# Performance work log

Hardware: AMD Instinct MI355X
Metric: run time of the kernel (lower is better)

## Reference

```python
import jax, jax.numpy as jnp
import numpy as np

B, T, F, U = 256, 2048, 64, 64
KEEP = 0.5  # recurrent_dropout=0.5 -> keep prob 0.5


def setup_inputs() -> dict:
    key = jax.random.key(0)
    ks = jax.random.split(key, 7)
    inputs = jax.random.normal(ks[0], (B, T, F), dtype=jnp.float32)
    kernel = jax.random.normal(ks[1], (F, 3 * U), dtype=jnp.float32) * 0.1
    recurrent_kernel = jax.random.normal(ks[2], (U, 3 * U), dtype=jnp.float32) * 0.1
    bias = jax.random.normal(ks[3], (2, 3 * U), dtype=jnp.float32) * 0.1
    dense_w = jax.random.normal(ks[4], (U, 1), dtype=jnp.float32) * 0.1
    dense_b = jnp.zeros((1,), dtype=jnp.float32)
    # Keras recurrent dropout: one fixed mask per gate (z, r, h), constant over time,
    # applied to h_prev before the recurrent matmul; inverted-dropout scaling.
    bern = jax.random.bernoulli(ks[5], KEEP, (3, B, U)).astype(jnp.float32)
    rec_mask = bern / KEEP
    return {
        "inputs": inputs,
        "kernel": kernel,
        "recurrent_kernel": recurrent_kernel,
        "bias": bias,
        "dense_w": dense_w,
        "dense_b": dense_b,
        "rec_mask": rec_mask,
    }


def _gru_dense(inputs, kernel, recurrent_kernel, bias, dense_w, dense_b, rec_mask):
    # Precompute input projections for all timesteps: [B, T, 3U]
    x_proj = jnp.einsum("btf,fg->btg", inputs, kernel) + bias[0]
    Uz, Ur, Uh = jnp.split(recurrent_kernel, 3, axis=1)  # each [U, U]
    bz, br, bh = jnp.split(bias[1], 3)                   # each [U]
    mz, mr, mh = rec_mask[0], rec_mask[1], rec_mask[2]   # each [B, U]

    def step(h, xt):
        xz, xr, xh = jnp.split(xt, 3, axis=-1)  # each [B, U]
        z = jax.nn.sigmoid(xz + (h * mz) @ Uz + bz)
        r = jax.nn.sigmoid(xr + (h * mr) @ Ur + br)
        hh = jnp.tanh(xh + r * ((h * mh) @ Uh + bh))  # reset_after=True
        h_new = z * h + (1.0 - z) * hh
        return h_new, None

    h0 = jnp.zeros((B, U), dtype=inputs.dtype)
    h_last, _ = jax.lax.scan(step, h0, jnp.swapaxes(x_proj, 0, 1))  # scan over T
    return h_last @ dense_w + dense_b  # [B, 1]


def reference(inputs, kernel, recurrent_kernel, bias, dense_w, dense_b, rec_mask):
    return _gru_dense(inputs, kernel, recurrent_kernel, bias, dense_w, dense_b, rec_mask)
```

## Files before the change

### kernel.cpp

```cpp
#include <hip/hip_runtime.h>

#define BB 256
#define TT 2048
#define FF 64
#define UU 64
#define C3 192

__device__ __forceinline__ float readlane_f(float v, int lane) {
    return __int_as_float(__builtin_amdgcn_readlane(__float_as_int(v), lane));
}
__device__ __forceinline__ float fast_sigmoid(float x) {
    return __builtin_amdgcn_rcpf(1.0f + __expf(-x));
}
__device__ __forceinline__ float fast_tanh(float x) {
    return 1.0f - 2.0f * __builtin_amdgcn_rcpf(__expf(2.0f * x) + 1.0f);
}

#define REP16(M) M(0) M(1) M(2) M(3) M(4) M(5) M(6) M(7) \
                 M(8) M(9) M(10) M(11) M(12) M(13) M(14) M(15)

__global__ __launch_bounds__(256, 1)
void gru_coop(const float* __restrict__ in, const float* __restrict__ kmat,
              const float* __restrict__ rk, const float* __restrict__ bias,
              const float* __restrict__ mask, const float* __restrict__ dw,
              const float* __restrict__ db, float* __restrict__ out) {
    __shared__ float ps[2][4][64][5];
    const int b    = blockIdx.x;
    const int lane = threadIdx.x & 63;
    const int wv   = threadIdx.x >> 6;
    const int i0   = wv << 4;

    const float mzv = mask[(size_t)b * UU + lane];
    const float mrv = mask[(size_t)(BB * UU) + (size_t)b * UU + lane];
    const float mhv = mask[(size_t)(2 * BB * UU) + (size_t)b * UU + lane];

#define DECLW(I) float uz_##I, ur_##I, uh_##I, kz_##I, kr_##I, kh_##I;
    REP16(DECLW)
#define INITW(I) { const int i_ = i0 + (I); \
    uz_##I = rk[i_ * C3 + lane]        * readlane_f(mzv, i_); \
    ur_##I = rk[i_ * C3 + 64 + lane]   * readlane_f(mrv, i_); \
    uh_##I = rk[i_ * C3 + 128 + lane]  * readlane_f(mhv, i_); \
    kz_##I = kmat[i_ * C3 + lane]; \
    kr_##I = kmat[i_ * C3 + 64 + lane]; \
    kh_##I = kmat[i_ * C3 + 128 + lane]; }
    REP16(INITW)

    const float bzf = bias[lane]       + bias[C3 + lane];
    const float brf = bias[64 + lane]  + bias[C3 + 64 + lane];
    const float bh0 = bias[128 + lane];
    const float bh1 = bias[C3 + 128 + lane];

    const float* __restrict__ inb = in + (size_t)b * TT * FF;

    float a0 = inb[(size_t)0 * FF + lane];
    float a1 = inb[(size_t)1 * FF + lane];
    float a2 = inb[(size_t)2 * FF + lane];
    float a3 = inb[(size_t)3 * FF + lane];
    float n0, n1, n2, n3;

    float h = 0.0f;

#define ACC1(I, AV) { \
    const float hs_ = readlane_f(h,  i0 + (I)); \
    const float as_ = readlane_f(AV, i0 + (I)); \
    pz  = fmaf(hs_, uz_##I, pz);  pz  = fmaf(as_, kz_##I, pz); \
    pr  = fmaf(hs_, ur_##I, pr);  pr  = fmaf(as_, kr_##I, pr); \
    pah = fmaf(hs_, uh_##I, pah); pxh = fmaf(as_, kh_##I, pxh); }

#define SUBSTEP(S, AV, NV) { \
    const int t_ = (tb << 2) + (S); \
    { const int rn_ = (t_ + 4 < TT) ? (t_ + 4) : (TT - 1); \
      NV = inb[(size_t)rn_ * FF + lane]; } \
    float pz = 0.0f, pr = 0.0f, pxh = 0.0f, pah = 0.0f; \
    REP16(ACC_##AV) \
    float* wp_ = &ps[(S) & 1][wv][lane][0]; \
    wp_[0] = pz; wp_[1] = pr; wp_[2] = pxh; wp_[3] = pah; \
    __syncthreads(); \
    float sz = bzf, sr = brf, sxh = bh0, sah = bh1; \
    { const float* rp_ = &ps[(S) & 1][0][lane][0]; \
      sz += rp_[0];   sr += rp_[1];   sxh += rp_[2];   sah += rp_[3]; \
      sz += rp_[320]; sr += rp_[321]; sxh += rp_[322]; sah += rp_[323]; \
      sz += rp_[640]; sr += rp_[641]; sxh += rp_[642]; sah += rp_[643]; \
      sz += rp_[960]; sr += rp_[961]; sxh += rp_[962]; sah += rp_[963]; } \
    const float z_  = fast_sigmoid(sz); \
    const float r_  = fast_sigmoid(sr); \
    const float hh_ = fast_tanh(fmaf(r_, sah, sxh)); \
    h = fmaf(z_, h - hh_, hh_); }

#define ACC_a0(I) ACC1(I, a0)
#define ACC_a1(I) ACC1(I, a1)
#define ACC_a2(I) ACC1(I, a2)
#define ACC_a3(I) ACC1(I, a3)

#pragma unroll 1
    for (int tb = 0; tb < TT / 4; ++tb) {
        SUBSTEP(0, a0, n0)
        SUBSTEP(1, a1, n1)
        SUBSTEP(2, a2, n2)
        SUBSTEP(3, a3, n3)
        a0 = n0; a1 = n1; a2 = n2; a3 = n3;
    }

    if (wv == 0) {
        float p = h * dw[lane];
#pragma unroll
        for (int o = 32; o > 0; o >>= 1) p += __shfl_down(p, o, 64);
        if (lane == 0) out[b] = p + db[0];
    }
}

extern "C" void kernel_launch(void* const* d_in, const int* in_sizes, int n_in,
                              void* d_out, int out_size, void* d_ws, size_t ws_size,
                              hipStream_t stream) {
    const float* inputs = (const float*)d_in[0];
    const float* kmat   = (const float*)d_in[1];
    const float* rk     = (const float*)d_in[2];
    const float* bias   = (const float*)d_in[3];
    const float* dw     = (const float*)d_in[4];
    const float* db     = (const float*)d_in[5];
    const float* mask   = (const float*)d_in[6];
    float* out = (float*)d_out;

    gru_coop<<<BB, 256, 0, stream>>>(inputs, kmat, rk, bias, mask, dw, db, out);
}
```

Before: 939.6 us.

## Repartition GRU step by output units with shuffle reduction and LDS h broadcast

Each wave now owns 16 output units, and the 64 lanes split the 64-term contraction into four 16-term groups. Partials are combined with cross-lane xor shuffles instead of an LDS reduction, and the new hidden state is broadcast through a double-buffered LDS array read as float4. Inputs are prefetched by one wave into an LDS ring. The aim is to cut the per-step readlane chain and the LDS reduction traffic, at the cost of shuffle latency and an extra LDS read of h each step.

```diff
diff --git a/kernel.cpp b/kernel.cpp
--- a/kernel.cpp
+++ b/kernel.cpp
@@ -6,103 +6,130 @@
 #define UU 64
 #define C3 192
 
-__device__ __forceinline__ float readlane_f(float v, int lane) {
-    return __int_as_float(__builtin_amdgcn_readlane(__float_as_int(v), lane));
-}
 __device__ __forceinline__ float fast_sigmoid(float x) {
     return __builtin_amdgcn_rcpf(1.0f + __expf(-x));
 }
 __device__ __forceinline__ float fast_tanh(float x) {
     return 1.0f - 2.0f * __builtin_amdgcn_rcpf(__expf(2.0f * x) + 1.0f);
 }
+__device__ __forceinline__ float shflx(float v, int m) {
+    return __shfl_xor(v, m, 64);
+}
 
 #define REP16(M) M(0) M(1) M(2) M(3) M(4) M(5) M(6) M(7) \
                  M(8) M(9) M(10) M(11) M(12) M(13) M(14) M(15)
 
-__global__ __launch_bounds__(256, 1)
-void gru_coop(const float* __restrict__ in, const float* __restrict__ kmat,
-              const float* __restrict__ rk, const float* __restrict__ bias,
-              const float* __restrict__ mask, const float* __restrict__ dw,
-              const float* __restrict__ db, float* __restrict__ out) {
-    __shared__ float ps[2][4][64][5];
+__global__ void __launch_bounds__(256)
+__attribute__((amdgpu_waves_per_eu(1, 1)))
+gru_v4(const float* __restrict__ in, const float* __restrict__ kmat,
+       const float* __restrict__ rk, const float* __restrict__ bias,
+       const float* __restrict__ mask, const float* __restrict__ dw,
+       const float* __restrict__ db, float* __restrict__ out) {
+    __shared__ __align__(16) float hbuf[2][64];
+    __shared__ __align__(16) float abuf[8][64];
+
     const int b    = blockIdx.x;
     const int lane = threadIdx.x & 63;
     const int wv   = threadIdx.x >> 6;
-    const int i0   = wv << 4;
+    const int sub  = lane >> 4;
+    const int u    = lane & 15;
+    const int j    = wv * 16 + u;
+    const int i0   = sub * 16;
 
-    const float mzv = mask[(size_t)b * UU + lane];
-    const float mrv = mask[(size_t)(BB * UU) + (size_t)b * UU + lane];
-    const float mhv = mask[(size_t)(2 * BB * UU) + (size_t)b * UU + lane];
-
-#define DECLW(I) float uz_##I, ur_##I, uh_##I, kz_##I, kr_##I, kh_##I;
+    const float* mzp = mask;
+    const float* mrp = mask + (size_t)BB * UU;
+    const float* mhp = mask + (size_t)2 * BB * UU;
+#define DECLW(K) float uz##K, ur##K, uh##K, kz##K, kr##K, kh##K;
     REP16(DECLW)
-#define INITW(I) { const int i_ = i0 + (I); \
-    uz_##I = rk[i_ * C3 + lane]        * readlane_f(mzv, i_); \
-    ur_##I = rk[i_ * C3 + 64 + lane]   * readlane_f(mrv, i_); \
-    uh_##I = rk[i_ * C3 + 128 + lane]  * readlane_f(mhv, i_); \
-    kz_##I = kmat[i_ * C3 + lane]; \
-    kr_##I = kmat[i_ * C3 + 64 + lane]; \
-    kh_##I = kmat[i_ * C3 + 128 + lane]; }
+#define INITW(K) { const int i_ = i0 + (K); \
+    uz##K = rk[i_ * C3 + j]        * mzp[(size_t)b * UU + i_]; \
+    ur##K = rk[i_ * C3 + 64 + j]   * mrp[(size_t)b * UU + i_]; \
+    uh##K = rk[i_ * C3 + 128 + j]  * mhp[(size_t)b * UU + i_]; \
+    kz##K = kmat[i_ * C3 + j]; \
+    kr##K = kmat[i_ * C3 + 64 + j]; \
+    kh##K = kmat[i_ * C3 + 128 + j]; }
     REP16(INITW)
 
-    const float bzf = bias[lane]       + bias[C3 + lane];
-    const float brf = bias[64 + lane]  + bias[C3 + 64 + lane];
-    const float bh0 = bias[128 + lane];
-    const float bh1 = bias[C3 + 128 + lane];
+    const float bzj  = bias[j]       + bias[C3 + j];
+    const float brj  = bias[64 + j]  + bias[C3 + 64 + j];
+    const float bh0j = bias[128 + j];
+    const float bh1j = bias[C3 + 128 + j];
 
-    const float* __restrict__ inb = in + (size_t)b * TT * FF;
+    const float* __restrict__ inb = in + (size_t)b * TT * FF + lane;
 
-    float a0 = inb[(size_t)0 * FF + lane];
-    float a1 = inb[(size_t)1 * FF + lane];
-    float a2 = inb[(size_t)2 * FF + lane];
-    float a3 = inb[(size_t)3 * FF + lane];
-    float n0, n1, n2, n3;
+    float ga = 0.f, gb = 0.f;
+    if (wv == 0) {
+        const float t0v = inb[0];
+        const float t1v = inb[(size_t)1 * FF];
+        ga = inb[(size_t)2 * FF];
+        gb = inb[(size_t)3 * FF];
+        abuf[0][lane] = t0v;
+        abuf[1][lane] = t1v;
+        hbuf[0][lane] = 0.0f;
+    }
+    __syncthreads();
 
-    float h = 0.0f;
+    float4 aA = *(const float4*)&abuf[0][i0];
+    float4 aB = *(const float4*)&abuf[0][i0 + 4];
+    float4 aC = *(const float4*)&abuf[0][i0 + 8];
+    float4 aD = *(const float4*)&abuf[0][i0 + 12];
 
-#define ACC1(I, AV) { \
-    const float hs_ = readlane_f(h,  i0 + (I)); \
-    const float as_ = readlane_f(AV, i0 + (I)); \
-    pz  = fmaf(hs_, uz_##I, pz);  pz  = fmaf(as_, kz_##I, pz); \
-    pr  = fmaf(hs_, ur_##I, pr);  pr  = fmaf(as_, kr_##I, pr); \
-    pah = fmaf(hs_, uh_##I, pah); pxh = fmaf(as_, kh_##I, pxh); }
-
-#define SUBSTEP(S, AV, NV) { \
-    const int t_ = (tb << 2) + (S); \
-    { const int rn_ = (t_ + 4 < TT) ? (t_ + 4) : (TT - 1); \
-      NV = inb[(size_t)rn_ * FF + lane]; } \
-    float pz = 0.0f, pr = 0.0f, pxh = 0.0f, pah = 0.0f; \
-    REP16(ACC_##AV) \
-    float* wp_ = &ps[(S) & 1][wv][lane][0]; \
-    wp_[0] = pz; wp_[1] = pr; wp_[2] = pxh; wp_[3] = pah; \
-    __syncthreads(); \
-    float sz = bzf, sr = brf, sxh = bh0, sah = bh1; \
-    { const float* rp_ = &ps[(S) & 1][0][lane][0]; \
-      sz += rp_[0];   sr += rp_[1];   sxh += rp_[2];   sah += rp_[3]; \
-      sz += rp_[320]; sr += rp_[321]; sxh += rp_[322]; sah += rp_[323]; \
-      sz += rp_[640]; sr += rp_[641]; sxh += rp_[642]; sah += rp_[643]; \
-      sz += rp_[960]; sr += rp_[961]; sxh += rp_[962]; sah += rp_[963]; } \
-    const float z_  = fast_sigmoid(sz); \
-    const float r_  = fast_sigmoid(sr); \
-    const float hh_ = fast_tanh(fmaf(r_, sah, sxh)); \
-    h = fmaf(z_, h - hh_, hh_); }
-
-#define ACC_a0(I) ACC1(I, a0)
-#define ACC_a1(I) ACC1(I, a1)
-#define ACC_a2(I) ACC1(I, a2)
-#define ACC_a3(I) ACC1(I, a3)
+    float hown = 0.0f;
 
 #pragma unroll 1
-    for (int tb = 0; tb < TT / 4; ++tb) {
-        SUBSTEP(0, a0, n0)
-        SUBSTEP(1, a1, n1)
-        SUBSTEP(2, a2, n2)
-        SUBSTEP(3, a3, n3)
-        a0 = n0; a1 = n1; a2 = n2; a3 = n3;
+    for (int e = 0; e < TT; ++e) {
+        const float4 hA = *(const float4*)&hbuf[e & 1][i0];
+        const float4 hB = *(const float4*)&hbuf[e & 1][i0 + 4];
+        const float4 hC = *(const float4*)&hbuf[e & 1][i0 + 8];
+        const float4 hD = *(const float4*)&hbuf[e & 1][i0 + 12];
+
+        float az = 0.f, ar = 0.f, axh = 0.f;
+#define FMA_A(K, AV) { az = fmaf(AV, kz##K, az); ar = fmaf(AV, kr##K, ar); \
+                       axh = fmaf(AV, kh##K, axh); }
+        FMA_A(0, aA.x)  FMA_A(1, aA.y)  FMA_A(2, aA.z)  FMA_A(3, aA.w)
+        FMA_A(4, aB.x)  FMA_A(5, aB.y)  FMA_A(6, aB.z)  FMA_A(7, aB.w)
+        FMA_A(8, aC.x)  FMA_A(9, aC.y)  FMA_A(10, aC.z) FMA_A(11, aC.w)
+        FMA_A(12, aD.x) FMA_A(13, aD.y) FMA_A(14, aD.z) FMA_A(15, aD.w)
+
+        float hz = 0.f, hr = 0.f, hah = 0.f;
+#define FMA_H(K, HV) { hz = fmaf(HV, uz##K, hz); hr = fmaf(HV, ur##K, hr); \
+                       hah = fmaf(HV, uh##K, hah); }
+        FMA_H(0, hA.x)  FMA_H(1, hA.y)  FMA_H(2, hA.z)  FMA_H(3, hA.w)
+        FMA_H(4, hB.x)  FMA_H(5, hB.y)  FMA_H(6, hB.z)  FMA_H(7, hB.w)
+        FMA_H(8, hC.x)  FMA_H(9, hC.y)  FMA_H(10, hC.z) FMA_H(11, hC.w)
+        FMA_H(12, hD.x) FMA_H(13, hD.y) FMA_H(14, hD.z) FMA_H(15, hD.w)
+
+        float sz = az + hz, sr = ar + hr, sxh = axh, sah = hah;
+        { float t0 = shflx(sz, 16), t1 = shflx(sr, 16),
+                t2 = shflx(sxh, 16), t3 = shflx(sah, 16);
+          sz += t0; sr += t1; sxh += t2; sah += t3; }
+        { float t0 = shflx(sz, 32), t1 = shflx(sr, 32),
+                t2 = shflx(sxh, 32), t3 = shflx(sah, 32);
+          sz += t0; sr += t1; sxh += t2; sah += t3; }
+
+        const float z  = fast_sigmoid(sz + bzj);
+        const float r  = fast_sigmoid(sr + brj);
+        const float hh = fast_tanh(fmaf(r, sah + bh1j, sxh + bh0j));
+        hown = fmaf(z, hown - hh, hh);
+
+        if (sub == 0) hbuf[(e + 1) & 1][j] = hown;
+        if (wv == 0) {
+            if (e + 2 < TT) abuf[(e + 2) & 7][lane] = ga;
+            ga = gb;
+            if (e + 4 < TT) gb = inb[(size_t)(e + 4) * FF];
+        }
+        __syncthreads();
+
+        if (e + 1 < TT) {
+            aA = *(const float4*)&abuf[(e + 1) & 7][i0];
+            aB = *(const float4*)&abuf[(e + 1) & 7][i0 + 4];
+            aC = *(const float4*)&abuf[(e + 1) & 7][i0 + 8];
+            aD = *(const float4*)&abuf[(e + 1) & 7][i0 + 12];
+        }
     }
 
     if (wv == 0) {
-        float p = h * dw[lane];
+        float p = hbuf[0][lane] * dw[lane];
 #pragma unroll
         for (int o = 32; o > 0; o >>= 1) p += __shfl_down(p, o, 64);
         if (lane == 0) out[b] = p + db[0];
@@ -112,6 +139,7 @@
 extern "C" void kernel_launch(void* const* d_in, const int* in_sizes, int n_in,
                               void* d_out, int out_size, void* d_ws, size_t ws_size,
                               hipStream_t stream) {
+    (void)in_sizes; (void)n_in; (void)d_ws; (void)ws_size; (void)out_size;
     const float* inputs = (const float*)d_in[0];
     const float* kmat   = (const float*)d_in[1];
     const float* rk     = (const float*)d_in[2];
@@ -121,5 +149,5 @@
     const float* mask   = (const float*)d_in[6];
     float* out = (float*)d_out;
 
-    gru_coop<<<BB, 256, 0, stream>>>(inputs, kmat, rk, bias, mask, dw, db, out);
+    gru_v4<<<BB, 256, 0, stream>>>(inputs, kmat, rk, bias, mask, dw, db, out);
 }
```

Result: slower. 1.489 ms (+58.5%).

## Software-pipeline input projection off the critical path with LDS chunk staging

Applied to the files above, without the earlier changes.

Each step's input-projection FMAs for the next timestep now run after the barrier, overlapping the partial-sum reduction and gate math, so only the recurrent h FMAs sit before the barrier. Input rows are staged into a double-buffered LDS chunk of 32 timesteps with batched global loads, replacing per-step global loads. Mask values are read directly instead of via readlane. This shortens the serial dependency chain per step, but adds LDS traffic, more registers and branchy staging code.

```diff
diff --git a/kernel.cpp b/kernel.cpp
--- a/kernel.cpp
+++ b/kernel.cpp
@@ -5,6 +5,8 @@
 #define FF 64
 #define UU 64
 #define C3 192
+#define CH 32
+#define NCH (TT / CH)
 
 __device__ __forceinline__ float readlane_f(float v, int lane) {
     return __int_as_float(__builtin_amdgcn_readlane(__float_as_int(v), lane));
@@ -19,30 +21,33 @@
 #define REP16(M) M(0) M(1) M(2) M(3) M(4) M(5) M(6) M(7) \
                  M(8) M(9) M(10) M(11) M(12) M(13) M(14) M(15)
 
-__global__ __launch_bounds__(256, 1)
-void gru_coop(const float* __restrict__ in, const float* __restrict__ kmat,
-              const float* __restrict__ rk, const float* __restrict__ bias,
-              const float* __restrict__ mask, const float* __restrict__ dw,
-              const float* __restrict__ db, float* __restrict__ out) {
+__global__ void __launch_bounds__(256)
+__attribute__((amdgpu_waves_per_eu(1, 1)))
+gru_v5(const float* __restrict__ in, const float* __restrict__ kmat,
+       const float* __restrict__ rk, const float* __restrict__ bias,
+       const float* __restrict__ mask, const float* __restrict__ dw,
+       const float* __restrict__ db, float* __restrict__ out) {
     __shared__ float ps[2][4][64][5];
+    __shared__ float abuf[2][CH][FF];
+
     const int b    = blockIdx.x;
     const int lane = threadIdx.x & 63;
     const int wv   = threadIdx.x >> 6;
     const int i0   = wv << 4;
 
-    const float mzv = mask[(size_t)b * UU + lane];
-    const float mrv = mask[(size_t)(BB * UU) + (size_t)b * UU + lane];
-    const float mhv = mask[(size_t)(2 * BB * UU) + (size_t)b * UU + lane];
+    const float* mzp = mask;
+    const float* mrp = mask + (size_t)BB * UU;
+    const float* mhp = mask + (size_t)2 * BB * UU;
 
-#define DECLW(I) float uz_##I, ur_##I, uh_##I, kz_##I, kr_##I, kh_##I;
+#define DECLW(K) float uz##K, ur##K, uh##K, kz##K, kr##K, kh##K;
     REP16(DECLW)
-#define INITW(I) { const int i_ = i0 + (I); \
-    uz_##I = rk[i_ * C3 + lane]        * readlane_f(mzv, i_); \
-    ur_##I = rk[i_ * C3 + 64 + lane]   * readlane_f(mrv, i_); \
-    uh_##I = rk[i_ * C3 + 128 + lane]  * readlane_f(mhv, i_); \
-    kz_##I = kmat[i_ * C3 + lane]; \
-    kr_##I = kmat[i_ * C3 + 64 + lane]; \
-    kh_##I = kmat[i_ * C3 + 128 + lane]; }
+#define INITW(K) { const int i_ = i0 + (K); \
+    uz##K = rk[i_ * C3 + lane]        * mzp[(size_t)b * UU + i_]; \
+    ur##K = rk[i_ * C3 + 64 + lane]   * mrp[(size_t)b * UU + i_]; \
+    uh##K = rk[i_ * C3 + 128 + lane]  * mhp[(size_t)b * UU + i_]; \
+    kz##K = kmat[i_ * C3 + lane]; \
+    kr##K = kmat[i_ * C3 + 64 + lane]; \
+    kh##K = kmat[i_ * C3 + 128 + lane]; }
     REP16(INITW)
 
     const float bzf = bias[lane]       + bias[C3 + lane];
@@ -52,53 +57,83 @@
 
     const float* __restrict__ inb = in + (size_t)b * TT * FF;
 
-    float a0 = inb[(size_t)0 * FF + lane];
-    float a1 = inb[(size_t)1 * FF + lane];
-    float a2 = inb[(size_t)2 * FF + lane];
-    float a3 = inb[(size_t)3 * FF + lane];
-    float n0, n1, n2, n3;
+    {
+        const float* src = inb + (size_t)(wv * 8) * FF + lane;
+        const float t0 = src[0 * FF], t1 = src[1 * FF], t2 = src[2 * FF],
+                    t3 = src[3 * FF], t4 = src[4 * FF], t5 = src[5 * FF],
+                    t6 = src[6 * FF], t7 = src[7 * FF];
+        float* dst = &abuf[0][wv * 8][lane];
+        dst[0 * FF] = t0; dst[1 * FF] = t1; dst[2 * FF] = t2; dst[3 * FF] = t3;
+        dst[4 * FF] = t4; dst[5 * FF] = t5; dst[6 * FF] = t6; dst[7 * FF] = t7;
+    }
+    __syncthreads();
 
+    float az_p = 0.f, ar_p = 0.f, axh_p = 0.f;
+    {
+        const float a0 = abuf[0][0][lane];
+#define FMA_A0(K) { const float s_ = readlane_f(a0, i0 + (K)); \
+        az_p = fmaf(s_, kz##K, az_p); ar_p = fmaf(s_, kr##K, ar_p); \
+        axh_p = fmaf(s_, kh##K, axh_p); }
+        REP16(FMA_A0)
+    }
+    float a_cur = abuf[0][1][lane];
     float h = 0.0f;
 
-#define ACC1(I, AV) { \
-    const float hs_ = readlane_f(h,  i0 + (I)); \
-    const float as_ = readlane_f(AV, i0 + (I)); \
-    pz  = fmaf(hs_, uz_##I, pz);  pz  = fmaf(as_, kz_##I, pz); \
-    pr  = fmaf(hs_, ur_##I, pr);  pr  = fmaf(as_, kr_##I, pr); \
-    pah = fmaf(hs_, uh_##I, pah); pxh = fmaf(as_, kh_##I, pxh); }
+#pragma unroll 1
+    for (int t = 0; t < TT; ++t) {
+        float pz = az_p, pr = ar_p, pxh = axh_p, pah = 0.f;
+#define FMA_H(K) { const float hs_ = readlane_f(h, i0 + (K)); \
+        pz  = fmaf(hs_, uz##K, pz); pr = fmaf(hs_, ur##K, pr); \
+        pah = fmaf(hs_, uh##K, pah); }
+        REP16(FMA_H)
 
-#define SUBSTEP(S, AV, NV) { \
-    const int t_ = (tb << 2) + (S); \
-    { const int rn_ = (t_ + 4 < TT) ? (t_ + 4) : (TT - 1); \
-      NV = inb[(size_t)rn_ * FF + lane]; } \
-    float pz = 0.0f, pr = 0.0f, pxh = 0.0f, pah = 0.0f; \
-    REP16(ACC_##AV) \
-    float* wp_ = &ps[(S) & 1][wv][lane][0]; \
-    wp_[0] = pz; wp_[1] = pr; wp_[2] = pxh; wp_[3] = pah; \
-    __syncthreads(); \
-    float sz = bzf, sr = brf, sxh = bh0, sah = bh1; \
-    { const float* rp_ = &ps[(S) & 1][0][lane][0]; \
-      sz += rp_[0];   sr += rp_[1];   sxh += rp_[2];   sah += rp_[3]; \
-      sz += rp_[320]; sr += rp_[321]; sxh += rp_[322]; sah += rp_[323]; \
-      sz += rp_[640]; sr += rp_[641]; sxh += rp_[642]; sah += rp_[643]; \
-      sz += rp_[960]; sr += rp_[961]; sxh += rp_[962]; sah += rp_[963]; } \
-    const float z_  = fast_sigmoid(sz); \
-    const float r_  = fast_sigmoid(sr); \
-    const float hh_ = fast_tanh(fmaf(r_, sah, sxh)); \
-    h = fmaf(z_, h - hh_, hh_); }
+        {
+            float* wp = &ps[t & 1][wv][lane][0];
+            wp[0] = pz; wp[1] = pr; wp[2] = pxh; wp[3] = pah;
+        }
+        __syncthreads();
 
-#define ACC_a0(I) ACC1(I, a0)
-#define ACC_a1(I) ACC1(I, a1)
-#define ACC_a2(I) ACC1(I, a2)
-#define ACC_a3(I) ACC1(I, a3)
+        const int  c        = t >> 5;
+        const bool do_stage = ((t & (CH - 1)) == 0) && (c + 1 < NCH);
+        float g0, g1, g2, g3, g4, g5, g6, g7;
+        if (do_stage) {
+            const float* src = inb + ((size_t)(c + 1) * CH + wv * 8) * FF + lane;
+            g0 = src[0 * FF]; g1 = src[1 * FF]; g2 = src[2 * FF]; g3 = src[3 * FF];
+            g4 = src[4 * FF]; g5 = src[5 * FF]; g6 = src[6 * FF]; g7 = src[7 * FF];
+        }
 
-#pragma unroll 1
-    for (int tb = 0; tb < TT / 4; ++tb) {
-        SUBSTEP(0, a0, n0)
-        SUBSTEP(1, a1, n1)
-        SUBSTEP(2, a2, n2)
-        SUBSTEP(3, a3, n3)
-        a0 = n0; a1 = n1; a2 = n2; a3 = n3;
+        const float* rp = &ps[t & 1][0][lane][0];
+        const float q00 = rp[0],   q01 = rp[1],   q02 = rp[2],   q03 = rp[3];
+        const float q10 = rp[320], q11 = rp[321], q12 = rp[322], q13 = rp[323];
+        const float q20 = rp[640], q21 = rp[641], q22 = rp[642], q23 = rp[643];
+        const float q30 = rp[960], q31 = rp[961], q32 = rp[962], q33 = rp[963];
+
+        float azn = 0.f, arn = 0.f, axhn = 0.f;
+#define FMA_AN(K) { const float s_ = readlane_f(a_cur, i0 + (K)); \
+        azn = fmaf(s_, kz##K, azn); arn = fmaf(s_, kr##K, arn); \
+        axhn = fmaf(s_, kh##K, axhn); }
+        REP16(FMA_AN)
+
+        const int rn = (t + 2 < TT) ? (t + 2) : (TT - 1);
+        const float a_next = abuf[(rn >> 5) & 1][rn & (CH - 1)][lane];
+
+        const float sz  = ((bzf + q00) + (q10 + q20)) + q30;
+        const float sr  = ((brf + q01) + (q11 + q21)) + q31;
+        const float sxh = ((bh0 + q02) + (q12 + q22)) + q32;
+        const float sah = ((bh1 + q03) + (q13 + q23)) + q33;
+        const float z  = fast_sigmoid(sz);
+        const float r  = fast_sigmoid(sr);
+        const float hh = fast_tanh(fmaf(r, sah, sxh));
+        h = fmaf(z, h - hh, hh);
+
+        if (do_stage) {
+            float* dst = &abuf[(c + 1) & 1][wv * 8][lane];
+            dst[0 * FF] = g0; dst[1 * FF] = g1; dst[2 * FF] = g2; dst[3 * FF] = g3;
+            dst[4 * FF] = g4; dst[5 * FF] = g5; dst[6 * FF] = g6; dst[7 * FF] = g7;
+        }
+
+        az_p = azn; ar_p = arn; axh_p = axhn;
+        a_cur = a_next;
     }
 
     if (wv == 0) {
@@ -112,6 +147,7 @@
 extern "C" void kernel_launch(void* const* d_in, const int* in_sizes, int n_in,
                               void* d_out, int out_size, void* d_ws, size_t ws_size,
                               hipStream_t stream) {
+    (void)in_sizes; (void)n_in; (void)d_ws; (void)ws_size; (void)out_size;
     const float* inputs = (const float*)d_in[0];
     const float* kmat   = (const float*)d_in[1];
     const float* rk     = (const float*)d_in[2];
@@ -121,5 +157,5 @@
     const float* mask   = (const float*)d_in[6];
     float* out = (float*)d_out;
 
-    gru_coop<<<BB, 256, 0, stream>>>(inputs, kmat, rk, bias, mask, dw, db, out);
+    gru_v5<<<BB, 256, 0, stream>>>(inputs, kmat, rk, bias, mask, dw, db, out);
 }
```

After: 1.469 ms. 1.56x slower.
